# Kernel optimization log

Hardware: AMD Instinct MI355X
Metric: run time of the kernel (lower is better)

Reference implementation:

```python
import jax, jax.numpy as jnp
import numpy as np

B, L = 4, 2048
D_MODEL, D_STATE, D_CONV, N_BLOCKS = 128, 16, 8, 6
EXPAND = 2
D_INNER = EXPAND * D_MODEL          # 256
DT_RANK = (D_MODEL + 15) // 16      # 8
CONV_K = 7                          # pre_conv kernel


def setup_inputs() -> dict:
    key = jax.random.key(0)
    ks = jax.random.split(key, 10)
    f = lambda k, s: jax.random.normal(k, s, jnp.float32)
    sc = 0.02
    A_init = jnp.broadcast_to(
        jnp.log(jnp.arange(1, D_STATE + 1, dtype=jnp.float32)),
        (N_BLOCKS, D_INNER, D_STATE)) + 0.0
    return {
        "x": f(ks[0], (B, L, 1)),
        "pre_conv_w": f(ks[1], (D_MODEL, 1, CONV_K)) * sc,
        "pre_conv_b": jnp.zeros((D_MODEL,), jnp.float32),
        "ln_w": jnp.ones((N_BLOCKS, D_MODEL), jnp.float32),
        "ln_b": jnp.zeros((N_BLOCKS, D_MODEL), jnp.float32),
        "W_in": f(ks[2], (N_BLOCKS, 2 * D_INNER, D_MODEL)) * sc,
        "conv_w": f(ks[3], (N_BLOCKS, D_INNER, 1, D_CONV)) * sc,  # depthwise OIH
        "conv_b": jnp.zeros((N_BLOCKS, D_INNER), jnp.float32),
        "W_x": f(ks[4], (N_BLOCKS, DT_RANK + 2 * D_STATE, D_INNER)) * sc,
        "W_dt": f(ks[5], (N_BLOCKS, D_INNER, DT_RANK)) * sc,
        "b_dt": jnp.full((N_BLOCKS, D_INNER), -4.6, jnp.float32),  # softplus ~ 0.01
        "A_log": A_init,
        "D_skip": jnp.ones((N_BLOCKS, D_INNER), jnp.float32),
        "W_out": f(ks[6], (N_BLOCKS, D_MODEL, D_INNER)) * sc,
        "out_w": f(ks[7], (1, D_MODEL)) * sc,
        "out_b": jnp.zeros((1,), jnp.float32),
    }


def _layernorm(x, w, b, eps=1e-5):
    m = jnp.mean(x, axis=-1, keepdims=True)
    v = jnp.mean(jnp.square(x - m), axis=-1, keepdims=True)
    return (x - m) * jax.lax.rsqrt(v + eps) * w + b


def _mamba(x, W_in, cw, cb, W_x, W_dt, b_dt, A_log, D_skip, W_out):
    # x: (B, L, D_MODEL)
    xz = jnp.einsum('bld,ed->ble', x, W_in)            # (B,L,2E)
    xi, z = jnp.split(xz, 2, axis=-1)
    # depthwise causal conv over time
    xc = jax.lax.conv_general_dilated(
        xi.transpose(0, 2, 1), cw, window_strides=(1,),
        padding=[(D_CONV - 1, 0)],
        dimension_numbers=('NCH', 'OIH', 'NCH'),
        feature_group_count=D_INNER) + cb[None, :, None]
    xc = jax.nn.silu(xc).transpose(0, 2, 1)            # (B,L,E)
    dbl = jnp.einsum('ble,re->blr', xc, W_x)
    dt = dbl[..., :DT_RANK]
    Bm = dbl[..., DT_RANK:DT_RANK + D_STATE]           # (B,L,N)
    Cm = dbl[..., DT_RANK + D_STATE:]                  # (B,L,N)
    delta = jax.nn.softplus(jnp.einsum('blr,er->ble', dt, W_dt) + b_dt)
    A = -jnp.exp(A_log)                                # (E,N)

    def step(h, inp):
        d, b, c, u = inp                               # (B,E),(B,N),(B,N),(B,E)
        h = h * jnp.exp(d[..., None] * A) + (d * u)[..., None] * b[:, None, :]
        return h, jnp.einsum('ben,bn->be', h, c)

    h0 = jnp.zeros((x.shape[0], D_INNER, D_STATE), x.dtype)
    xs = (delta.transpose(1, 0, 2), Bm.transpose(1, 0, 2),
          Cm.transpose(1, 0, 2), xc.transpose(1, 0, 2))
    _, ys = jax.lax.scan(step, h0, xs)                 # ys: (L,B,E)
    y = ys.transpose(1, 0, 2) + D_skip * xc
    y = y * jax.nn.silu(z)
    return jnp.einsum('ble,de->bld', y, W_out)


def reference(x, pre_conv_w, pre_conv_b, ln_w, ln_b, W_in, conv_w, conv_b,
              W_x, W_dt, b_dt, A_log, D_skip, W_out, out_w, out_b):
    # pre_conv (1 -> d_model), SAME padding, then exact GELU
    h = jax.lax.conv_general_dilated(
        x.transpose(0, 2, 1), pre_conv_w, window_strides=(1,),
        padding=[(CONV_K // 2, CONV_K // 2)],
        dimension_numbers=('NCH', 'OIH', 'NCH')) + pre_conv_b[None, :, None]
    h = jax.nn.gelu(h, approximate=False).transpose(0, 2, 1)  # (B,L,D)

    def block(carry, p):
        lw, lb, Wi, cw, cb, Wx, Wdt, bdt, Alog, Dsk, Wo = p
        y = _mamba(_layernorm(carry, lw, lb), Wi, cw, cb, Wx, Wdt, bdt, Alog, Dsk, Wo)
        return carry + y, None                         # dropout is identity (eval)

    h, _ = jax.lax.scan(block, h, (ln_w, ln_b, W_in, conv_w, conv_b,
                                   W_x, W_dt, b_dt, A_log, D_skip, W_out))
    return (jnp.einsum('bld,od->blo', h, out_w) + out_b)[..., 0]  # (B,L)
```

## Files before the change

kernel.cpp:

```cpp
#include <hip/hip_runtime.h>
#include <hip/hip_bf16.h>
#include <hip/hip_cooperative_groups.h>
#include <math.h>

namespace cg = cooperative_groups;

#define BB 4
#define LL 2048
#define DM 128
#define DI 256
#define DS 16
#define DTR 8
#define NB 6
#define KPRE 7
#define KC 8
#define NC 128
#define CT 16
#define NCHUNK (BB*NC)
#define BL (BB*LL)
#define SU 4

typedef __attribute__((ext_vector_type(8))) short short8v;
typedef __attribute__((ext_vector_type(4))) short short4v;
typedef __attribute__((ext_vector_type(4))) float f32x4;

__device__ __forceinline__ void store_bf16x4(__hip_bfloat16* p, float a, float b, float c, float d) {
    __hip_bfloat16 t[4] = {__float2bfloat16(a), __float2bfloat16(b),
                           __float2bfloat16(c), __float2bfloat16(d)};
    *(short4v*)p = *(const short4v*)t;
}
__device__ __forceinline__ float4 load_bf16x4(const __hip_bfloat16* p) {
    short4v raw = *(const short4v*)p;
    const __hip_bfloat16* t = (const __hip_bfloat16*)&raw;
    return make_float4(__bfloat162float(t[0]), __bfloat162float(t[1]),
                       __bfloat162float(t[2]), __bfloat162float(t[3]));
}
__device__ __forceinline__ void load_bf16x8(const __hip_bfloat16* p, float* o) {
    short8v a = *(const short8v*)p;
    const __hip_bfloat16* ta = (const __hip_bfloat16*)&a;
#pragma unroll
    for (int i = 0; i < 8; ++i) o[i] = __bfloat162float(ta[i]);
}
__device__ __forceinline__ void store_bf16x8(__hip_bfloat16* p, const float* v) {
    __hip_bfloat16 t[8];
#pragma unroll
    for (int i = 0; i < 8; ++i) t[i] = __float2bfloat16(v[i]);
    *(short8v*)p = *(const short8v*)t;
}


__device__ __forceinline__ void dev_preconv(int idx,
    const float* __restrict__ x, const float* __restrict__ w, const float* __restrict__ bias,
    float* __restrict__ h, const float* __restrict__ Wi, const float* __restrict__ Wo,
    const float* __restrict__ Wxf,
    __hip_bfloat16* __restrict__ wi, __hip_bfloat16* __restrict__ wo,
    __hip_bfloat16* __restrict__ wx) {
    int d = idx & (DM - 1);
    int l = (idx >> 7) & (LL - 1);
    int b = idx >> 18;
    float acc = bias[d];
#pragma unroll
    for (int k = 0; k < KPRE; ++k) {
        int pos = l + k - 3;
        float xv = (pos >= 0 && pos < LL) ? x[b * LL + pos] : 0.f;
        acc = fmaf(xv, w[d * KPRE + k], acc);
    }
    h[idx] = 0.5f * acc * (1.f + erff(acc * 0.70710678118654752f));
    if (idx < NB * 2 * DI * DM) wi[idx] = __float2bfloat16(Wi[idx]);
    if (idx < NB * DM * DI)     wo[idx] = __float2bfloat16(Wo[idx]);
    if (idx < NB * 40 * DI)     wx[idx] = __float2bfloat16(Wxf[idx]);
}

__device__ __forceinline__ void dev_phaseA(int chunk, int tid, int epoch,
    const float* __restrict__ h, const float* __restrict__ lw, const float* __restrict__ lb,
    const __hip_bfloat16* __restrict__ Wi, const __hip_bfloat16* __restrict__ Wx,
    const float* __restrict__ cw, const float* __restrict__ cbs,
    const float* __restrict__ Wdt, const float* __restrict__ bdt,
    const float* __restrict__ A_log,
    __hip_bfloat16* __restrict__ Pst, __hip_bfloat16* __restrict__ hend,
    __hip_bfloat16* __restrict__ hincl, int* __restrict__ flags,
    __hip_bfloat16* As, __hip_bfloat16 (*xi_s)[DI],
    __hip_bfloat16 (*xcb_s)[DI], float (*dl_s)[DI], float (*bc_s)[32],
    __hip_bfloat16 (*z_s)[DI], __hip_bfloat16 (*hin_s)[DS], float (*dbl_s)[48]) {
    int c = chunk & (NC - 1);
    int b = chunk >> 7;
    int wave = tid >> 6, lane = tid & 63;
    for (int it = 0; it < 4; ++it) {
        int lr = wave * 4 + it;
        int tl = c * CT + lr - 16;
        int sw = (lr & 7) << 3;
        if (tl >= 0) {
            int t = b * LL + tl;
            float v0 = h[t * DM + lane];
            float v1 = h[t * DM + lane + 64];
            float s = v0 + v1;
#pragma unroll
            for (int off = 32; off; off >>= 1) s += __shfl_xor(s, off);
            float mean = s * (1.f / 128.f);
            float d0 = v0 - mean, d1 = v1 - mean;
            float q = d0 * d0 + d1 * d1;
#pragma unroll
            for (int off = 32; off; off >>= 1) q += __shfl_xor(q, off);
            float rstd = rsqrtf(q * (1.f / 128.f) + 1e-5f);
            As[lr * 128 + (lane ^ sw)]        = __float2bfloat16(d0 * rstd * lw[lane] + lb[lane]);
            As[lr * 128 + ((lane + 64) ^ sw)] = __float2bfloat16(d1 * rstd * lw[lane + 64] + lb[lane + 64]);
        } else {
            As[lr * 128 + (lane ^ sw)]        = __float2bfloat16(0.f);
            As[lr * 128 + ((lane + 64) ^ sw)] = __float2bfloat16(0.f);
        }
    }
    __syncthreads();
    {
        int r = lane & 15, kh = lane >> 4;
        short8v af[2][4];
#pragma unroll
        for (int mf = 0; mf < 2; ++mf)
#pragma unroll
            for (int k = 0; k < 4; ++k) {
                int row = mf * 16 + r;
                int cbk = k * 4 + kh;
                af[mf][k] = *(const short8v*)&As[row * 128 + ((cbk ^ (row & 7)) << 3)];
            }
        if (wave < 4) {
            int nBase = wave * 64;
            for (int nf = 0; nf < 4; ++nf) {
                short8v bfr[4];
#pragma unroll
                for (int k = 0; k < 4; ++k)
                    bfr[k] = *(const short8v*)&Wi[(size_t)(nBase + nf * 16 + r) * DM + k * 32 + kh * 8];
                f32x4 acc0 = {}, acc1 = {};
#pragma unroll
                for (int k = 0; k < 4; ++k) {
                    acc0 = __builtin_amdgcn_mfma_f32_16x16x32_bf16(af[0][k], bfr[k], acc0, 0, 0, 0);
                    acc1 = __builtin_amdgcn_mfma_f32_16x16x32_bf16(af[1][k], bfr[k], acc1, 0, 0, 0);
                }
#pragma unroll
                for (int rg = 0; rg < 4; ++rg) {
                    xi_s[kh * 4 + rg][nBase + nf * 16 + r]      = __float2bfloat16(acc0[rg]);
                    xi_s[16 + kh * 4 + rg][nBase + nf * 16 + r] = __float2bfloat16(acc1[rg]);
                }
            }
        } else {
            int zBase = (wave - 4) * 64;
            for (int nf = 0; nf < 4; ++nf) {
                short8v bfr[4];
#pragma unroll
                for (int k = 0; k < 4; ++k)
                    bfr[k] = *(const short8v*)&Wi[(size_t)(256 + zBase + nf * 16 + r) * DM + k * 32 + kh * 8];
                f32x4 acc1 = {};
#pragma unroll
                for (int k = 0; k < 4; ++k)
                    acc1 = __builtin_amdgcn_mfma_f32_16x16x32_bf16(af[1][k], bfr[k], acc1, 0, 0, 0);
#pragma unroll
                for (int rg = 0; rg < 4; ++rg)
                    z_s[kh * 4 + rg][zBase + nf * 16 + r] = __float2bfloat16(acc1[rg]);
            }
        }
    }
    __syncthreads();
    for (int i = 0; i < 2; ++i) {
        int lt = wave * 2 + i;
#pragma unroll
        for (int j = 0; j < 4; ++j) {
            int e = lane + 64 * j;
            float4 c0 = *(const float4*)&cw[e * KC];
            float4 c1 = *(const float4*)&cw[e * KC + 4];
            float wts[8] = {c0.x, c0.y, c0.z, c0.w, c1.x, c1.y, c1.z, c1.w};
            float acc = cbs[e];
#pragma unroll
            for (int k = 0; k < KC; ++k)
                acc = fmaf(__bfloat162float(xi_s[lt + 9 + k][e]), wts[k], acc);
            float sv = acc / (1.f + __expf(-acc));
            xcb_s[lt][e] = __float2bfloat16(sv);
        }
    }
    __syncthreads();
    if (wave < 3) {
        int r = lane & 15, kh = lane >> 4;
        f32x4 acc = {};
        for (int k0 = 0; k0 < DI; k0 += 32) {
            short8v a = *(const short8v*)&xcb_s[r][k0 + kh * 8];
            int o = wave * 16 + r;
            short8v w8;
            if (o < 40) w8 = *(const short8v*)&Wx[(size_t)o * DI + k0 + kh * 8];
            else { short z[8] = {}; w8 = *(const short8v*)z; }
            acc = __builtin_amdgcn_mfma_f32_16x16x32_bf16(a, w8, acc, 0, 0, 0);
        }
#pragma unroll
        for (int rg = 0; rg < 4; ++rg)
            dbl_s[kh * 4 + rg][wave * 16 + r] = acc[rg];
    }
    __syncthreads();
    {
        int l = tid >> 5, i = tid & 31;
        bc_s[l][i] = dbl_s[l][8 + i];
    }
    {
        int e = tid & 255, th = tid >> 8;
        for (int l = th * 8; l < th * 8 + 8; ++l) {
            float s = bdt[e];
#pragma unroll
            for (int r = 0; r < 8; ++r) s = fmaf(dbl_s[l][r], Wdt[e * 8 + r], s);
            dl_s[l][e] = fmaxf(s, 0.f) + log1pf(__expf(-fabsf(s)));
        }
    }
    __syncthreads();
    int e = tid >> 1, half = tid & 1;
    for (int ngi = 0; ngi < 2; ++ngi) {
        int ng = half * 2 + ngi;
        float4 al = *(const float4*)&A_log[e * DS + 4 * ng];
        float Aen[4] = {-__expf(al.x), -__expf(al.y), -__expf(al.z), -__expf(al.w)};
        float hh[4] = {}, Pl[4] = {1.f, 1.f, 1.f, 1.f};
#pragma unroll
        for (int l = 0; l < CT; ++l) {
            float dv = dl_s[l][e];
            float uv = __bfloat162float(xcb_s[l][e]);
            float du = dv * uv;
            float4 bm = *(const float4*)&bc_s[l][4 * ng];
            float a0 = __expf(dv * Aen[0]);
            float a1 = __expf(dv * Aen[1]);
            float a2 = __expf(dv * Aen[2]);
            float a3 = __expf(dv * Aen[3]);
            hh[0] = fmaf(hh[0], a0, du * bm.x);
            hh[1] = fmaf(hh[1], a1, du * bm.y);
            hh[2] = fmaf(hh[2], a2, du * bm.z);
            hh[3] = fmaf(hh[3], a3, du * bm.w);
            Pl[0] *= a0; Pl[1] *= a1; Pl[2] *= a2; Pl[3] *= a3;
        }
        size_t oidx = (((size_t)(b * NC + c)) * DI + e) * DS + 4 * ng;
        store_bf16x4(&Pst[oidx], Pl[0], Pl[1], Pl[2], Pl[3]);
        store_bf16x4(&hend[oidx], hh[0], hh[1], hh[2], hh[3]);
    }
    __threadfence();
    __syncthreads();
    if (tid == 0)
        __hip_atomic_store(&flags[b * NC + c], 2 * epoch,
                           __ATOMIC_RELEASE, __HIP_MEMORY_SCOPE_AGENT);
    float hacc[8], Pacc[8];
#pragma unroll
    for (int n = 0; n < 8; ++n) { hacc[n] = 0.f; Pacc[n] = 1.f; }
    int j = c - 1;
    while (j >= 0) {
        int f1;
        do {
            f1 = __hip_atomic_load(&flags[b * NC + j], __ATOMIC_ACQUIRE, __HIP_MEMORY_SCOPE_AGENT);
            if (f1 < 2 * epoch) __builtin_amdgcn_s_sleep(2);
        } while (f1 < 2 * epoch);
        size_t bj = (((size_t)(b * NC + j)) * DI + e) * DS + half * 8;
        if (f1 > 2 * epoch) {
            float hi[8]; load_bf16x8(&hincl[bj], hi);
#pragma unroll
            for (int n = 0; n < 8; ++n) hacc[n] = fmaf(Pacc[n], hi[n], hacc[n]);
            break;
        }
        float pj[8], he[8];
        load_bf16x8(&Pst[bj], pj);
        load_bf16x8(&hend[bj], he);
#pragma unroll
        for (int n = 0; n < 8; ++n) { hacc[n] = fmaf(Pacc[n], he[n], hacc[n]); Pacc[n] *= pj[n]; }
        --j;
    }
    {
        size_t bcx = (((size_t)(b * NC + c)) * DI + e) * DS + half * 8;
        float pc[8], hc[8];
        load_bf16x8(&Pst[bcx], pc);
        load_bf16x8(&hend[bcx], hc);
#pragma unroll
        for (int n = 0; n < 8; ++n) {
            hin_s[e][half * 8 + n] = __float2bfloat16(hacc[n]);
            hc[n] = fmaf(pc[n], hacc[n], hc[n]);
        }
        store_bf16x8(&hincl[bcx], hc);
    }
    __threadfence();
    __syncthreads();
    if (tid == 0)
        __hip_atomic_store(&flags[b * NC + c], 2 * epoch + 1,
                           __ATOMIC_RELEASE, __HIP_MEMORY_SCOPE_AGENT);
}

__device__ __forceinline__ void dev_fusedB(int chunk, int tid,
    const float* __restrict__ A_log, const float* __restrict__ Dsk,
    const __hip_bfloat16* __restrict__ Wo, float* __restrict__ hout,
    const __hip_bfloat16 (*xcb_s)[DI], const float (*dl_s)[DI], const float (*bc_s)[32],
    const __hip_bfloat16 (*z_s)[DI], const __hip_bfloat16 (*hin_s)[DS],
    __hip_bfloat16 (*y_s)[DI + 8]) {
    int c = chunk & (NC - 1);
    int b = chunk >> 7;
    int base = b * LL + c * CT;
    int e = tid >> 1, half = tid & 1;
    float yacc[CT];
    float dsk = Dsk[e];
#pragma unroll
    for (int l = 0; l < CT; ++l)
        yacc[l] = half ? 0.f : dsk * __bfloat162float(xcb_s[l][e]);
    for (int ngi = 0; ngi < 2; ++ngi) {
        int ng = half * 2 + ngi;
        float4 al = *(const float4*)&A_log[e * DS + 4 * ng];
        float Aen[4] = {-__expf(al.x), -__expf(al.y), -__expf(al.z), -__expf(al.w)};
        float hh[4] = {__bfloat162float(hin_s[e][4 * ng]),
                       __bfloat162float(hin_s[e][4 * ng + 1]),
                       __bfloat162float(hin_s[e][4 * ng + 2]),
                       __bfloat162float(hin_s[e][4 * ng + 3])};
#pragma unroll
        for (int l = 0; l < CT; ++l) {
            float dv = dl_s[l][e];
            float uv = __bfloat162float(xcb_s[l][e]);
            float du = dv * uv;
            float4 bm = *(const float4*)&bc_s[l][4 * ng];
            float4 cm = *(const float4*)&bc_s[l][16 + 4 * ng];
            float a0 = __expf(dv * Aen[0]);
            float a1 = __expf(dv * Aen[1]);
            float a2 = __expf(dv * Aen[2]);
            float a3 = __expf(dv * Aen[3]);
            hh[0] = fmaf(hh[0], a0, du * bm.x);
            hh[1] = fmaf(hh[1], a1, du * bm.y);
            hh[2] = fmaf(hh[2], a2, du * bm.z);
            hh[3] = fmaf(hh[3], a3, du * bm.w);
            float p = hh[0] * cm.x;
            p = fmaf(hh[1], cm.y, p);
            p = fmaf(hh[2], cm.z, p);
            p = fmaf(hh[3], cm.w, p);
            yacc[l] += p;
        }
    }
#pragma unroll
    for (int l = 0; l < CT; ++l) {
        float full = yacc[l] + __shfl_xor(yacc[l], 1);
        if (half == 0) {
            float z = __bfloat162float(z_s[l][e]);
            y_s[l][e] = __float2bfloat16(full * (z / (1.f + __expf(-z))));
        }
    }
    __syncthreads();
    int wave = tid >> 6, lane = tid & 63;
    int r  = lane & 15;
    int kh = lane >> 4;
    f32x4 acc = {};
    for (int k0 = 0; k0 < DI; k0 += 32) {
        short8v af = *(const short8v*)&y_s[r][k0 + kh * 8];
        short8v bf = *(const short8v*)&Wo[(size_t)(wave * 16 + r) * DI + k0 + kh * 8];
        acc = __builtin_amdgcn_mfma_f32_16x16x32_bf16(af, bf, acc, 0, 0, 0);
    }
    __syncthreads();
#pragma unroll
    for (int rg = 0; rg < 4; ++rg) {
        size_t off = (size_t)(base + kh * 4 + rg) * DM + wave * 16 + r;
        hout[off] += acc[rg];
    }
}

__device__ __forceinline__ void dev_out(int t, int lane,
    const float* __restrict__ h, const float* __restrict__ ow, const float* __restrict__ ob,
    float* __restrict__ out) {
    float s = h[t * DM + lane] * ow[lane] + h[t * DM + lane + 64] * ow[lane + 64];
#pragma unroll
    for (int off = 32; off; off >>= 1) s += __shfl_xor(s, off);
    if (lane == 0) out[t] = s + ob[0];
}


struct MegaArgs {
    const float *x, *pcw, *pcb, *ln_w, *ln_b, *conv_w, *conv_b;
    const float *W_x, *W_dt, *b_dt, *A_log, *D_skip, *W_in, *W_out, *out_w, *out_b;
    float *h, *out;
    __hip_bfloat16 *P, *hend, *hincl, *wi_bf, *wo_bf, *wx_bf;
    int *flags;
};

__global__ __launch_bounds__(512, 4) void k_mega(MegaArgs a) {
    __shared__ union {
        struct {
            __hip_bfloat16 As[32 * 128];
            __hip_bfloat16 xi[32][DI];
        } pa;
        __hip_bfloat16 y_s[CT][DI + 8];
    } u;
    __shared__ __hip_bfloat16 xcb_s[CT][DI];
    __shared__ float dl_s[CT][DI];
    __shared__ float bc_s[CT][32];
    __shared__ __hip_bfloat16 z_s[CT][DI];
    __shared__ __hip_bfloat16 hin_s[DI][DS];
    __shared__ float dbl_s[CT][48];
    cg::grid_group g = cg::this_grid();
    int bid = blockIdx.x, tid = threadIdx.x;
    int nb = gridDim.x;
    int wave = tid >> 6, lane = tid & 63;

    for (int v = bid * 512 + tid; v < NCHUNK; v += nb * 512) a.flags[v] = 0;
    for (int v = bid; v < (BB * LL * DM) / 512; v += nb)
        dev_preconv(v * 512 + tid, a.x, a.pcw, a.pcb, a.h, a.W_in, a.W_out, a.W_x,
                    a.wi_bf, a.wo_bf, a.wx_bf);
    g.sync();

    for (int blk = 0; blk < NB; ++blk) {
        dev_phaseA(bid, tid, blk + 1, a.h, a.ln_w + blk * DM, a.ln_b + blk * DM,
                   a.wi_bf + (size_t)blk * 2 * DI * DM, a.wx_bf + (size_t)blk * 40 * DI,
                   a.conv_w + (size_t)blk * DI * KC, a.conv_b + blk * DI,
                   a.W_dt + (size_t)blk * DI * DTR, a.b_dt + blk * DI,
                   a.A_log + (size_t)blk * DI * DS,
                   a.P, a.hend, a.hincl, a.flags,
                   u.pa.As, u.pa.xi, xcb_s, dl_s, bc_s, z_s, hin_s, dbl_s);
        dev_fusedB(bid, tid, a.A_log + (size_t)blk * DI * DS,
                   a.D_skip + blk * DI, a.wo_bf + (size_t)blk * DM * DI, a.h,
                   xcb_s, dl_s, bc_s, z_s, hin_s, u.y_s);
        g.sync();
    }

    for (int v = bid; v < BL / 8; v += nb)
        dev_out(v * 8 + wave, lane, a.h, a.out_w, a.out_b, a.out);
}


__global__ void w_preconv(const float* x, const float* w, const float* bias, float* h,
                          const float* Wi, const float* Wo, const float* Wxf,
                          __hip_bfloat16* wi, __hip_bfloat16* wo, __hip_bfloat16* wx) {
    int idx = blockIdx.x * 256 + threadIdx.x;
    int d = idx & (DM - 1);
    int l = (idx >> 7) & (LL - 1);
    int b = idx >> 18;
    float acc = bias[d];
#pragma unroll
    for (int k = 0; k < KPRE; ++k) {
        int pos = l + k - 3;
        float xv = (pos >= 0 && pos < LL) ? x[b * LL + pos] : 0.f;
        acc = fmaf(xv, w[d * KPRE + k], acc);
    }
    h[idx] = 0.5f * acc * (1.f + erff(acc * 0.70710678118654752f));
    if (idx < NB * 2 * DI * DM) wi[idx] = __float2bfloat16(Wi[idx]);
    if (idx < NB * DM * DI)     wo[idx] = __float2bfloat16(Wo[idx]);
    if (idx < NB * 40 * DI)     wx[idx] = __float2bfloat16(Wxf[idx]);
}

__global__ __launch_bounds__(256) void w_ln_gemm1(const float* __restrict__ h,
    const float* __restrict__ lw, const float* __restrict__ lb,
    const __hip_bfloat16* __restrict__ W, float* __restrict__ xz) {
    __shared__ __hip_bfloat16 As[64 * 128];
    int v = blockIdx.x, wave = threadIdx.x >> 6, lane = threadIdx.x & 63;
    int tileM = v >> 2, tileN = v & 3;
    int mBase = tileM * 64, nBase = tileN * 128;
    for (int it = 0; it < 16; ++it) {
        int row = wave * 16 + it;
        int t = mBase + row;
        float v0 = h[t * DM + lane];
        float v1 = h[t * DM + lane + 64];
        float s = v0 + v1;
#pragma unroll
        for (int off = 32; off; off >>= 1) s += __shfl_xor(s, off);
        float mean = s * (1.f / 128.f);
        float d0 = v0 - mean, d1 = v1 - mean;
        float q = d0 * d0 + d1 * d1;
#pragma unroll
        for (int off = 32; off; off >>= 1) q += __shfl_xor(q, off);
        float rstd = rsqrtf(q * (1.f / 128.f) + 1e-5f);
        int sw = (row & 7) << 3;
        As[row * 128 + (lane ^ sw)]        = __float2bfloat16(d0 * rstd * lw[lane] + lb[lane]);
        As[row * 128 + ((lane + 64) ^ sw)] = __float2bfloat16(d1 * rstd * lw[lane + 64] + lb[lane + 64]);
    }
    __syncthreads();
    int r  = lane & 15;
    int kh = lane >> 4;
    f32x4 acc[4][2] = {};
    for (int k0 = 0; k0 < DM; k0 += 32) {
        short8v af[4], bf[2];
#pragma unroll
        for (int i = 0; i < 4; ++i) {
            int row = i * 16 + r;
            int cbk = (k0 >> 3) + kh;
            af[i] = *(const short8v*)&As[row * 128 + ((cbk ^ (row & 7)) << 3)];
        }
#pragma unroll
        for (int j = 0; j < 2; ++j)
            bf[j] = *(const short8v*)&W[(size_t)(nBase + wave * 32 + j * 16 + r) * DM + k0 + kh * 8];
#pragma unroll
        for (int i = 0; i < 4; ++i)
#pragma unroll
            for (int j = 0; j < 2; ++j)
                acc[i][j] = __builtin_amdgcn_mfma_f32_16x16x32_bf16(af[i], bf[j], acc[i][j], 0, 0, 0);
    }
#pragma unroll
    for (int i = 0; i < 4; ++i)
#pragma unroll
        for (int j = 0; j < 2; ++j)
#pragma unroll
            for (int rg = 0; rg < 4; ++rg) {
                size_t off = (size_t)(mBase + i * 16 + kh * 4 + rg) * (2 * DI)
                           + nBase + wave * 32 + j * 16 + r;
                xz[off] = acc[i][j][rg];
            }
}

__global__ __launch_bounds__(256) void w_conv_wx(const float* __restrict__ xz,
    const float* __restrict__ cw, const float* __restrict__ cbs,
    const float* __restrict__ Wx, const float* __restrict__ Wdt, const float* __restrict__ bdt,
    float* __restrict__ xc, float* __restrict__ BC, float* __restrict__ delta) {
    int lane = threadIdx.x & 63;
    int t = blockIdx.x * 4 + (threadIdx.x >> 6);
    int tl = t & (LL - 1);
    int b = t >> 11;
    float xv[4];
#pragma unroll
    for (int j = 0; j < 4; ++j) {
        int e = lane + 64 * j;
        float4 cw0 = *(const float4*)&cw[e * KC];
        float4 cw1 = *(const float4*)&cw[e * KC + 4];
        float wts[8] = {cw0.x, cw0.y, cw0.z, cw0.w, cw1.x, cw1.y, cw1.z, cw1.w};
        float acc = cbs[e];
#pragma unroll
        for (int k = 0; k < KC; ++k) {
            int pos = tl + k - (KC - 1);
            float v = (pos >= 0) ? xz[((size_t)(b * LL + pos) << 9) + e] : 0.f;
            acc = fmaf(v, wts[k], acc);
        }
        xv[j] = acc / (1.f + __expf(-acc));
        xc[((size_t)t << 8) + e] = xv[j];
    }
    float dt[8];
    float bcv = 0.f;
#pragma unroll
    for (int o = 0; o < 40; ++o) {
        const float* w = &Wx[o * DI];
        float s = xv[0] * w[lane];
        s = fmaf(xv[1], w[lane + 64], s);
        s = fmaf(xv[2], w[lane + 128], s);
        s = fmaf(xv[3], w[lane + 192], s);
#pragma unroll
        for (int off = 32; off; off >>= 1) s += __shfl_xor(s, off);
        if (o < 8) dt[o] = s;
        else if (lane == o - 8) bcv = s;
    }
    if (lane < 32) BC[((size_t)t << 5) + lane] = bcv;
#pragma unroll
    for (int j = 0; j < 4; ++j) {
        int e = lane + 64 * j;
        float s = bdt[e];
#pragma unroll
        for (int r = 0; r < 8; ++r) s = fmaf(dt[r], Wdt[e * 8 + r], s);
        delta[((size_t)t << 8) + e] = fmaxf(s, 0.f) + log1pf(__expf(-fabsf(s)));
    }
}

__global__ __launch_bounds__(256) void w_scan1(const float* __restrict__ delta,
    const float* __restrict__ xc, const float* __restrict__ BC,
    const float* __restrict__ A_log,
    __hip_bfloat16* __restrict__ P, __hip_bfloat16* __restrict__ hend) {
    int blk = blockIdx.x, tid = threadIdx.x;
    int eg = blk & 3;
    int c = (blk >> 2) & (NC - 1);
    int b = blk >> 9;
    int e = eg * 64 + (tid >> 2);
    int ng = tid & 3;
    float4 al = *(const float4*)&A_log[e * DS + 4 * ng];
    float Aen[4] = {-__expf(al.x), -__expf(al.y), -__expf(al.z), -__expf(al.w)};
    float h[4] = {}, Pl[4] = {1.f, 1.f, 1.f, 1.f};
    int base = b * LL + c * CT;
    const float* dp = delta + (size_t)base * DI + e;
    const float* up = xc + (size_t)base * DI + e;
    const float* bp = BC + (size_t)base * 32 + 4 * ng;
    for (int l0 = 0; l0 < CT; l0 += SU) {
        float d[SU], uu[SU];
        float4 bm[SU];
#pragma unroll
        for (int j = 0; j < SU; ++j) {
            d[j]  = dp[(l0 + j) * DI];
            uu[j] = up[(l0 + j) * DI];
            bm[j] = *(const float4*)&bp[(l0 + j) * 32];
        }
#pragma unroll
        for (int j = 0; j < SU; ++j) {
            float du = d[j] * uu[j];
            float a0 = __expf(d[j] * Aen[0]);
            float a1 = __expf(d[j] * Aen[1]);
            float a2 = __expf(d[j] * Aen[2]);
            float a3 = __expf(d[j] * Aen[3]);
            h[0] = fmaf(h[0], a0, du * bm[j].x);
            h[1] = fmaf(h[1], a1, du * bm[j].y);
            h[2] = fmaf(h[2], a2, du * bm[j].z);
            h[3] = fmaf(h[3], a3, du * bm[j].w);
            Pl[0] *= a0; Pl[1] *= a1; Pl[2] *= a2; Pl[3] *= a3;
        }
    }
    size_t oidx = (((size_t)(b * NC + c)) * DI + e) * DS + 4 * ng;
    store_bf16x4(&P[oidx], Pl[0], Pl[1], Pl[2], Pl[3]);
    store_bf16x4(&hend[oidx], h[0], h[1], h[2], h[3]);
}

__global__ void w_carry(const __hip_bfloat16* __restrict__ P,
                        const __hip_bfloat16* __restrict__ hend,
                        __hip_bfloat16* __restrict__ hin) {
    int gtid = blockIdx.x * 256 + threadIdx.x;
    int n = gtid & 15;
    int e = (gtid >> 4) & 255;
    int b = gtid >> 12;
    const size_t cs = (size_t)DI * DS;
    size_t idx0 = (((size_t)(b * NC)) * DI + e) * DS + n;
    float carry = 0.f;
    for (int c0 = 0; c0 < NC; c0 += 8) {
        float p[8], he[8];
#pragma unroll
        for (int j = 0; j < 8; ++j) {
            size_t idx = idx0 + (size_t)(c0 + j) * cs;
            p[j]  = __bfloat162float(P[idx]);
            he[j] = __bfloat162float(hend[idx]);
        }
#pragma unroll
        for (int j = 0; j < 8; ++j) {
            hin[idx0 + (size_t)(c0 + j) * cs] = __float2bfloat16(carry);
            carry = fmaf(p[j], carry, he[j]);
        }
    }
}

__global__ __launch_bounds__(256) void w_scan3(const float* __restrict__ delta,
    const float* __restrict__ xc, const float* __restrict__ BC,
    const float* __restrict__ A_log, const __hip_bfloat16* __restrict__ hin,
    const float* __restrict__ xz,
    const float* __restrict__ Dsk, __hip_bfloat16* __restrict__ y) {
    int blk = blockIdx.x, tid = threadIdx.x;
    int eg = blk & 3;
    int c = (blk >> 2) & (NC - 1);
    int b = blk >> 9;
    int e = eg * 64 + (tid >> 2);
    int ng = tid & 3;
    float4 al = *(const float4*)&A_log[e * DS + 4 * ng];
    float Aen[4] = {-__expf(al.x), -__expf(al.y), -__expf(al.z), -__expf(al.w)};
    float dsk = Dsk[e];
    float4 h4 = load_bf16x4(&hin[(((size_t)(b * NC + c)) * DI + e) * DS + 4 * ng]);
    float h[4] = {h4.x, h4.y, h4.z, h4.w};
    int base = b * LL + c * CT;
    const float* dp = delta + (size_t)base * DI + e;
    const float* up = xc + (size_t)base * DI + e;
    const float* bp = BC + (size_t)base * 32 + 4 * ng;
    const float* zp = xz + ((size_t)base << 9) + DI + e;
    __hip_bfloat16* yp = y + (size_t)base * DI + e;
    for (int l0 = 0; l0 < CT; l0 += SU) {
        float d[SU], uu[SU], zv[SU];
        float4 bm[SU], cm[SU];
#pragma unroll
        for (int j = 0; j < SU; ++j) {
            d[j]  = dp[(l0 + j) * DI];
            uu[j] = up[(l0 + j) * DI];
            bm[j] = *(const float4*)&bp[(l0 + j) * 32];
            cm[j] = *(const float4*)&bp[(l0 + j) * 32 + 16];
            zv[j] = zp[(size_t)(l0 + j) << 9];
        }
#pragma unroll
        for (int j = 0; j < SU; ++j) {
            float du = d[j] * uu[j];
            float a0 = __expf(d[j] * Aen[0]);
            float a1 = __expf(d[j] * Aen[1]);
            float a2 = __expf(d[j] * Aen[2]);
            float a3 = __expf(d[j] * Aen[3]);
            h[0] = fmaf(h[0], a0, du * bm[j].x);
            h[1] = fmaf(h[1], a1, du * bm[j].y);
            h[2] = fmaf(h[2], a2, du * bm[j].z);
            h[3] = fmaf(h[3], a3, du * bm[j].w);
            float yc = h[0] * cm[j].x;
            yc = fmaf(h[1], cm[j].y, yc);
            yc = fmaf(h[2], cm[j].z, yc);
            yc = fmaf(h[3], cm[j].w, yc);
            yc += __shfl_xor(yc, 1);
            yc += __shfl_xor(yc, 2);
            if (ng == 0) {
                float z = zv[j];
                float val = (yc + dsk * uu[j]) * (z / (1.f + __expf(-z)));
                yp[(l0 + j) * DI] = __float2bfloat16(val);
            }
        }
    }
}

__global__ __launch_bounds__(256) void w_gemm2(const __hip_bfloat16* __restrict__ A,
                                               const __hip_bfloat16* __restrict__ W,
                                               float* __restrict__ C) {
    int v = blockIdx.x, wave = threadIdx.x >> 6, lane = threadIdx.x & 63;
    int mBase = v * 16;
    int r  = lane & 15;
    int kh = lane >> 4;
    f32x4 acc[2] = {};
    for (int k0 = 0; k0 < DI; k0 += 32) {
        short8v af = *(const short8v*)&A[(size_t)(mBase + r) * DI + k0 + kh * 8];
        short8v bf[2];
#pragma unroll
        for (int j = 0; j < 2; ++j)
            bf[j] = *(const short8v*)&W[(size_t)(wave * 32 + j * 16 + r) * DI + k0 + kh * 8];
#pragma unroll
        for (int j = 0; j < 2; ++j)
            acc[j] = __builtin_amdgcn_mfma_f32_16x16x32_bf16(af, bf[j], acc[j], 0, 0, 0);
    }
#pragma unroll
    for (int j = 0; j < 2; ++j)
#pragma unroll
        for (int rg = 0; rg < 4; ++rg) {
            size_t off = (size_t)(mBase + kh * 4 + rg) * DM + wave * 32 + j * 16 + r;
            C[off] += acc[j][rg];
        }
}

__global__ void w_out(const float* h, const float* ow, const float* ob, float* out) {
    dev_out(blockIdx.x * 4 + (threadIdx.x >> 6), threadIdx.x & 63, h, ow, ob, out);
}

extern "C" void kernel_launch(void* const* d_in, const int* in_sizes, int n_in,
                              void* d_out, int out_size, void* d_ws, size_t ws_size,
                              hipStream_t stream) {
    (void)in_sizes; (void)n_in; (void)out_size; (void)ws_size;
    const float* x      = (const float*)d_in[0];
    const float* pcw    = (const float*)d_in[1];
    const float* pcb    = (const float*)d_in[2];
    const float* ln_w   = (const float*)d_in[3];
    const float* ln_b   = (const float*)d_in[4];
    const float* W_in   = (const float*)d_in[5];
    const float* conv_w = (const float*)d_in[6];
    const float* conv_b = (const float*)d_in[7];
    const float* W_x    = (const float*)d_in[8];
    const float* W_dt   = (const float*)d_in[9];
    const float* b_dt   = (const float*)d_in[10];
    const float* A_log  = (const float*)d_in[11];
    const float* D_skip = (const float*)d_in[12];
    const float* W_out  = (const float*)d_in[13];
    const float* out_w  = (const float*)d_in[14];
    const float* out_b  = (const float*)d_in[15];

    const size_t SCAN_N = (size_t)BB * NC * DI * DS;
    float* ws    = (float*)d_ws;
    float* h     = ws;
    float* xz    = h     + (size_t)BL * DM;
    float* xc    = xz    + (size_t)BL * 2 * DI;
    float* BC    = xc    + (size_t)BL * DI;
    float* delta = BC    + (size_t)BL * 2 * DS;
    __hip_bfloat16* P     = (__hip_bfloat16*)(delta + (size_t)BL * DI);
    __hip_bfloat16* hend  = P + SCAN_N;
    __hip_bfloat16* hin   = hend + SCAN_N;
    __hip_bfloat16* hincl = hin + SCAN_N;
    __hip_bfloat16* y_bf  = hincl + SCAN_N;
    __hip_bfloat16* wi_bf = y_bf + (size_t)BL * DI;
    __hip_bfloat16* wo_bf = wi_bf + (size_t)NB * 2 * DI * DM;
    __hip_bfloat16* wx_bf = wo_bf + (size_t)NB * DM * DI;
    int* flags = (int*)(wx_bf + (size_t)NB * 40 * DI);

    int dev = 0;
    (void)hipGetDevice(&dev);
    int coopAttr = 0;
    (void)hipDeviceGetAttribute(&coopAttr, hipDeviceAttributeCooperativeLaunch, dev);
    int numCU = 0;
    (void)hipDeviceGetAttribute(&numCU, hipDeviceAttributeMultiprocessorCount, dev);
    int maxBpCU = 0;
    (void)hipOccupancyMaxActiveBlocksPerMultiprocessor(&maxBpCU, k_mega, 512, 0);
    int grid = maxBpCU * numCU;
    if (grid > NCHUNK) grid = NCHUNK;

    bool launched = false;
    if (coopAttr && grid == NCHUNK) {
        MegaArgs ma = {x, pcw, pcb, ln_w, ln_b, conv_w, conv_b,
                       W_x, W_dt, b_dt, A_log, D_skip, W_in, W_out, out_w, out_b,
                       h, (float*)d_out,
                       P, hend, hincl, wi_bf, wo_bf, wx_bf, flags};
        void* kp[] = {&ma};
        hipError_t e = hipLaunchCooperativeKernel((void*)k_mega, dim3(grid), dim3(512), kp, 0, stream);
        launched = (e == hipSuccess);
        if (!launched) (void)hipGetLastError();
    }

    if (!launched) {
        w_preconv<<<(BB * LL * DM) / 256, 256, 0, stream>>>(
            x, pcw, pcb, h, W_in, W_out, W_x, wi_bf, wo_bf, wx_bf);
        for (int blk = 0; blk < NB; ++blk) {
            w_ln_gemm1<<<512, 256, 0, stream>>>(
                h, ln_w + blk * DM, ln_b + blk * DM, wi_bf + (size_t)blk * 2 * DI * DM, xz);
            w_conv_wx<<<BL / 4, 256, 0, stream>>>(
                xz, conv_w + (size_t)blk * DI * KC, conv_b + blk * DI,
                W_x + (size_t)blk * 40 * DI, W_dt + (size_t)blk * DI * DTR,
                b_dt + blk * DI, xc, BC, delta);
            w_scan1<<<BB * NC * 4, 256, 0, stream>>>(
                delta, xc, BC, A_log + (size_t)blk * DI * DS, P, hend);
            w_carry<<<(BB * DI * DS) / 256, 256, 0, stream>>>(P, hend, hin);
            w_scan3<<<BB * NC * 4, 256, 0, stream>>>(
                delta, xc, BC, A_log + (size_t)blk * DI * DS, hin, xz, D_skip + blk * DI, y_bf);
            w_gemm2<<<BL / 16, 256, 0, stream>>>(y_bf, wo_bf + (size_t)blk * DM * DI, h);
        }
        w_out<<<BL / 4, 256, 0, stream>>>(h, out_w, out_b, (float*)d_out);
    }
}
```

Before: 556.7 us.

## Halve mega-kernel block size and give each thread a full state row

Shrinks the cooperative mega-kernel from 512 to 256 threads per block and remaps every phase to match. The LayerNorm rows, GEMM N-tiles, conv timesteps and out-projection tiles per wave are doubled, and each thread now owns one inner channel with all 16 SSM states. The intent is to remove the half-split with its shuffle reduction, and to cut per-block barrier and launch-bound pressure. The cost is fewer waves per CU to hide latency, and a longer serial scan and carry loop per thread.

```diff
diff --git a/kernel.cpp b/kernel.cpp
--- a/kernel.cpp
+++ b/kernel.cpp
@@ -35,17 +35,20 @@
     return make_float4(__bfloat162float(t[0]), __bfloat162float(t[1]),
                        __bfloat162float(t[2]), __bfloat162float(t[3]));
 }
-__device__ __forceinline__ void load_bf16x8(const __hip_bfloat16* p, float* o) {
+__device__ __forceinline__ void load_bf16x16(const __hip_bfloat16* p, float* o) {
     short8v a = *(const short8v*)p;
+    short8v b = *(const short8v*)(p + 8);
     const __hip_bfloat16* ta = (const __hip_bfloat16*)&a;
-#pragma unroll
-    for (int i = 0; i < 8; ++i) o[i] = __bfloat162float(ta[i]);
-}
-__device__ __forceinline__ void store_bf16x8(__hip_bfloat16* p, const float* v) {
-    __hip_bfloat16 t[8];
-#pragma unroll
-    for (int i = 0; i < 8; ++i) t[i] = __float2bfloat16(v[i]);
+    const __hip_bfloat16* tb = (const __hip_bfloat16*)&b;
+#pragma unroll
+    for (int i = 0; i < 8; ++i) { o[i] = __bfloat162float(ta[i]); o[8 + i] = __bfloat162float(tb[i]); }
+}
+__device__ __forceinline__ void store_bf16x16(__hip_bfloat16* p, const float* v) {
+    __hip_bfloat16 t[16];
+#pragma unroll
+    for (int i = 0; i < 16; ++i) t[i] = __float2bfloat16(v[i]);
     *(short8v*)p = *(const short8v*)t;
+    *(short8v*)(p + 8) = *(const short8v*)(t + 8);
 }
 
 
@@ -85,8 +88,8 @@
     int c = chunk & (NC - 1);
     int b = chunk >> 7;
     int wave = tid >> 6, lane = tid & 63;
-    for (int it = 0; it < 4; ++it) {
-        int lr = wave * 4 + it;
+    for (int it = 0; it < 8; ++it) {
+        int lr = wave * 8 + it;
         int tl = c * CT + lr - 16;
         int sw = (lr & 7) << 3;
         if (tl >= 0) {
@@ -121,13 +124,13 @@
                 int cbk = k * 4 + kh;
                 af[mf][k] = *(const short8v*)&As[row * 128 + ((cbk ^ (row & 7)) << 3)];
             }
-        if (wave < 4) {
-            int nBase = wave * 64;
-            for (int nf = 0; nf < 4; ++nf) {
-                short8v bfr[4];
-#pragma unroll
-                for (int k = 0; k < 4; ++k)
-                    bfr[k] = *(const short8v*)&Wi[(size_t)(nBase + nf * 16 + r) * DM + k * 32 + kh * 8];
+        int nBase = wave * 128;
+        for (int nf = 0; nf < 8; ++nf) {
+            short8v bfr[4];
+#pragma unroll
+            for (int k = 0; k < 4; ++k)
+                bfr[k] = *(const short8v*)&Wi[(size_t)(nBase + nf * 16 + r) * DM + k * 32 + kh * 8];
+            if (wave < 2) {
                 f32x4 acc0 = {}, acc1 = {};
 #pragma unroll
                 for (int k = 0; k < 4; ++k) {
@@ -139,27 +142,20 @@
                     xi_s[kh * 4 + rg][nBase + nf * 16 + r]      = __float2bfloat16(acc0[rg]);
                     xi_s[16 + kh * 4 + rg][nBase + nf * 16 + r] = __float2bfloat16(acc1[rg]);
                 }
-            }
-        } else {
-            int zBase = (wave - 4) * 64;
-            for (int nf = 0; nf < 4; ++nf) {
-                short8v bfr[4];
-#pragma unroll
-                for (int k = 0; k < 4; ++k)
-                    bfr[k] = *(const short8v*)&Wi[(size_t)(256 + zBase + nf * 16 + r) * DM + k * 32 + kh * 8];
+            } else {
                 f32x4 acc1 = {};
 #pragma unroll
                 for (int k = 0; k < 4; ++k)
                     acc1 = __builtin_amdgcn_mfma_f32_16x16x32_bf16(af[1][k], bfr[k], acc1, 0, 0, 0);
 #pragma unroll
                 for (int rg = 0; rg < 4; ++rg)
-                    z_s[kh * 4 + rg][zBase + nf * 16 + r] = __float2bfloat16(acc1[rg]);
+                    z_s[kh * 4 + rg][(nBase - 256) + nf * 16 + r] = __float2bfloat16(acc1[rg]);
             }
         }
     }
     __syncthreads();
-    for (int i = 0; i < 2; ++i) {
-        int lt = wave * 2 + i;
+    for (int i = 0; i < 4; ++i) {
+        int lt = wave * 4 + i;
 #pragma unroll
         for (int j = 0; j < 4; ++j) {
             int e = lane + 64 * j;
@@ -183,7 +179,7 @@
             int o = wave * 16 + r;
             short8v w8;
             if (o < 40) w8 = *(const short8v*)&Wx[(size_t)o * DI + k0 + kh * 8];
-            else { short z[8] = {}; w8 = *(const short8v*)z; }
+            else { short zz[8] = {}; w8 = *(const short8v*)zz; }
             acc = __builtin_amdgcn_mfma_f32_16x16x32_bf16(a, w8, acc, 0, 0, 0);
         }
 #pragma unroll
@@ -192,12 +188,13 @@
     }
     __syncthreads();
     {
-        int l = tid >> 5, i = tid & 31;
-        bc_s[l][i] = dbl_s[l][8 + i];
+        int l = tid >> 4, i = tid & 15;
+        bc_s[l][i]      = dbl_s[l][8 + i];
+        bc_s[l][16 + i] = dbl_s[l][24 + i];
     }
     {
-        int e = tid & 255, th = tid >> 8;
-        for (int l = th * 8; l < th * 8 + 8; ++l) {
+        int e = tid;
+        for (int l = 0; l < CT; ++l) {
             float s = bdt[e];
 #pragma unroll
             for (int r = 0; r < 8; ++r) s = fmaf(dbl_s[l][r], Wdt[e * 8 + r], s);
@@ -205,9 +202,8 @@
         }
     }
     __syncthreads();
-    int e = tid >> 1, half = tid & 1;
-    for (int ngi = 0; ngi < 2; ++ngi) {
-        int ng = half * 2 + ngi;
+    int e = tid;
+    for (int ng = 0; ng < 4; ++ng) {
         float4 al = *(const float4*)&A_log[e * DS + 4 * ng];
         float Aen[4] = {-__expf(al.x), -__expf(al.y), -__expf(al.z), -__expf(al.w)};
         float hh[4] = {}, Pl[4] = {1.f, 1.f, 1.f, 1.f};
@@ -236,9 +232,9 @@
     if (tid == 0)
         __hip_atomic_store(&flags[b * NC + c], 2 * epoch,
                            __ATOMIC_RELEASE, __HIP_MEMORY_SCOPE_AGENT);
-    float hacc[8], Pacc[8];
-#pragma unroll
-    for (int n = 0; n < 8; ++n) { hacc[n] = 0.f; Pacc[n] = 1.f; }
+    float hacc[16], Pacc[16];
+#pragma unroll
+    for (int n = 0; n < 16; ++n) { hacc[n] = 0.f; Pacc[n] = 1.f; }
     int j = c - 1;
     while (j >= 0) {
         int f1;
@@ -246,31 +242,31 @@
             f1 = __hip_atomic_load(&flags[b * NC + j], __ATOMIC_ACQUIRE, __HIP_MEMORY_SCOPE_AGENT);
             if (f1 < 2 * epoch) __builtin_amdgcn_s_sleep(2);
         } while (f1 < 2 * epoch);
-        size_t bj = (((size_t)(b * NC + j)) * DI + e) * DS + half * 8;
+        size_t bj = (((size_t)(b * NC + j)) * DI + e) * DS;
         if (f1 > 2 * epoch) {
-            float hi[8]; load_bf16x8(&hincl[bj], hi);
-#pragma unroll
-            for (int n = 0; n < 8; ++n) hacc[n] = fmaf(Pacc[n], hi[n], hacc[n]);
+            float hi[16]; load_bf16x16(&hincl[bj], hi);
+#pragma unroll
+            for (int n = 0; n < 16; ++n) hacc[n] = fmaf(Pacc[n], hi[n], hacc[n]);
             break;
         }
-        float pj[8], he[8];
-        load_bf16x8(&Pst[bj], pj);
-        load_bf16x8(&hend[bj], he);
-#pragma unroll
-        for (int n = 0; n < 8; ++n) { hacc[n] = fmaf(Pacc[n], he[n], hacc[n]); Pacc[n] *= pj[n]; }
+        float pj[16], he[16];
+        load_bf16x16(&Pst[bj], pj);
+        load_bf16x16(&hend[bj], he);
+#pragma unroll
+        for (int n = 0; n < 16; ++n) { hacc[n] = fmaf(Pacc[n], he[n], hacc[n]); Pacc[n] *= pj[n]; }
         --j;
     }
     {
-        size_t bcx = (((size_t)(b * NC + c)) * DI + e) * DS + half * 8;
-        float pc[8], hc[8];
-        load_bf16x8(&Pst[bcx], pc);
-        load_bf16x8(&hend[bcx], hc);
-#pragma unroll
-        for (int n = 0; n < 8; ++n) {
-            hin_s[e][half * 8 + n] = __float2bfloat16(hacc[n]);
+        size_t bcx = (((size_t)(b * NC + c)) * DI + e) * DS;
+        float pc[16], hc[16];
+        load_bf16x16(&Pst[bcx], pc);
+        load_bf16x16(&hend[bcx], hc);
+#pragma unroll
+        for (int n = 0; n < 16; ++n) {
+            hin_s[e][n] = __float2bfloat16(hacc[n]);
             hc[n] = fmaf(pc[n], hacc[n], hc[n]);
         }
-        store_bf16x8(&hincl[bcx], hc);
+        store_bf16x16(&hincl[bcx], hc);
     }
     __threadfence();
     __syncthreads();
@@ -288,14 +284,13 @@
     int c = chunk & (NC - 1);
     int b = chunk >> 7;
     int base = b * LL + c * CT;
-    int e = tid >> 1, half = tid & 1;
+    int e = tid;
     float yacc[CT];
     float dsk = Dsk[e];
 #pragma unroll
     for (int l = 0; l < CT; ++l)
-        yacc[l] = half ? 0.f : dsk * __bfloat162float(xcb_s[l][e]);
-    for (int ngi = 0; ngi < 2; ++ngi) {
-        int ng = half * 2 + ngi;
+        yacc[l] = dsk * __bfloat162float(xcb_s[l][e]);
+    for (int ng = 0; ng < 4; ++ng) {
         float4 al = *(const float4*)&A_log[e * DS + 4 * ng];
         float Aen[4] = {-__expf(al.x), -__expf(al.y), -__expf(al.z), -__expf(al.w)};
         float hh[4] = {__bfloat162float(hin_s[e][4 * ng]),
@@ -326,28 +321,32 @@
     }
 #pragma unroll
     for (int l = 0; l < CT; ++l) {
-        float full = yacc[l] + __shfl_xor(yacc[l], 1);
-        if (half == 0) {
-            float z = __bfloat162float(z_s[l][e]);
-            y_s[l][e] = __float2bfloat16(full * (z / (1.f + __expf(-z))));
-        }
+        float z = __bfloat162float(z_s[l][e]);
+        y_s[l][e] = __float2bfloat16(yacc[l] * (z / (1.f + __expf(-z))));
     }
     __syncthreads();
     int wave = tid >> 6, lane = tid & 63;
     int r  = lane & 15;
     int kh = lane >> 4;
-    f32x4 acc = {};
+    f32x4 acc[2] = {};
     for (int k0 = 0; k0 < DI; k0 += 32) {
         short8v af = *(const short8v*)&y_s[r][k0 + kh * 8];
-        short8v bf = *(const short8v*)&Wo[(size_t)(wave * 16 + r) * DI + k0 + kh * 8];
-        acc = __builtin_amdgcn_mfma_f32_16x16x32_bf16(af, bf, acc, 0, 0, 0);
-    }
-    __syncthreads();
-#pragma unroll
-    for (int rg = 0; rg < 4; ++rg) {
-        size_t off = (size_t)(base + kh * 4 + rg) * DM + wave * 16 + r;
-        hout[off] += acc[rg];
-    }
+        short8v bf[2];
+#pragma unroll
+        for (int jj = 0; jj < 2; ++jj)
+            bf[jj] = *(const short8v*)&Wo[(size_t)(wave * 32 + jj * 16 + r) * DI + k0 + kh * 8];
+#pragma unroll
+        for (int jj = 0; jj < 2; ++jj)
+            acc[jj] = __builtin_amdgcn_mfma_f32_16x16x32_bf16(af, bf[jj], acc[jj], 0, 0, 0);
+    }
+    __syncthreads();
+#pragma unroll
+    for (int jj = 0; jj < 2; ++jj)
+#pragma unroll
+        for (int rg = 0; rg < 4; ++rg) {
+            size_t off = (size_t)(base + kh * 4 + rg) * DM + wave * 32 + jj * 16 + r;
+            hout[off] += acc[jj][rg];
+        }
 }
 
 __device__ __forceinline__ void dev_out(int t, int lane,
@@ -368,7 +367,7 @@
     int *flags;
 };
 
-__global__ __launch_bounds__(512, 4) void k_mega(MegaArgs a) {
+__global__ __launch_bounds__(256, 2) void k_mega(MegaArgs a) {
     __shared__ union {
         struct {
             __hip_bfloat16 As[32 * 128];
@@ -387,9 +386,9 @@
     int nb = gridDim.x;
     int wave = tid >> 6, lane = tid & 63;
 
-    for (int v = bid * 512 + tid; v < NCHUNK; v += nb * 512) a.flags[v] = 0;
-    for (int v = bid; v < (BB * LL * DM) / 512; v += nb)
-        dev_preconv(v * 512 + tid, a.x, a.pcw, a.pcb, a.h, a.W_in, a.W_out, a.W_x,
+    for (int v = bid * 256 + tid; v < NCHUNK; v += nb * 256) a.flags[v] = 0;
+    for (int v = bid; v < (BB * LL * DM) / 256; v += nb)
+        dev_preconv(v * 256 + tid, a.x, a.pcw, a.pcb, a.h, a.W_in, a.W_out, a.W_x,
                     a.wi_bf, a.wo_bf, a.wx_bf);
     g.sync();
 
@@ -407,8 +406,8 @@
         g.sync();
     }
 
-    for (int v = bid; v < BL / 8; v += nb)
-        dev_out(v * 8 + wave, lane, a.h, a.out_w, a.out_b, a.out);
+    for (int v = bid; v < BL / 4; v += nb)
+        dev_out(v * 4 + wave, lane, a.h, a.out_w, a.out_b, a.out);
 }
 
 
@@ -746,7 +745,7 @@
     int numCU = 0;
     (void)hipDeviceGetAttribute(&numCU, hipDeviceAttributeMultiprocessorCount, dev);
     int maxBpCU = 0;
-    (void)hipOccupancyMaxActiveBlocksPerMultiprocessor(&maxBpCU, k_mega, 512, 0);
+    (void)hipOccupancyMaxActiveBlocksPerMultiprocessor(&maxBpCU, k_mega, 256, 0);
     int grid = maxBpCU * numCU;
     if (grid > NCHUNK) grid = NCHUNK;
 
@@ -757,7 +756,7 @@
                        h, (float*)d_out,
                        P, hend, hincl, wi_bf, wo_bf, wx_bf, flags};
         void* kp[] = {&ma};
-        hipError_t e = hipLaunchCooperativeKernel((void*)k_mega, dim3(grid), dim3(512), kp, 0, stream);
+        hipError_t e = hipLaunchCooperativeKernel((void*)k_mega, dim3(grid), dim3(256), kp, 0, stream);
         launched = (e == hipSuccess);
         if (!launched) (void)hipGetLastError();
     }
```

After: 555.1 us. About the same (-0.3%).
